# Performance work log

Measured on AMD Instinct MI355X. Metric: run time of the kernel, lower is better.

Reference implementation:

```python
import jax, jax.numpy as jnp
import numpy as np

N_NODES = 50000
N_EDGES = 1600000
HIDDEN = 64
HEADS = 8
EPS = 1e-16  # matches PyG segment-softmax denominator epsilon


def setup_inputs() -> dict:
    key = jax.random.key(0)
    ks = jax.random.split(key, 8)
    node_features = jax.random.normal(ks[0], (N_NODES,), dtype=jnp.float32)
    edge_index = jax.random.randint(ks[1], (2, N_EDGES), 0, N_NODES, dtype=jnp.int64)
    cycle_mask = jax.random.uniform(ks[2], (N_EDGES,), dtype=jnp.float32)
    # feature_proj: Linear(1, HIDDEN)
    W_proj = jax.random.normal(ks[3], (HIDDEN, 1), dtype=jnp.float32) * 0.5
    b_proj = jax.random.normal(ks[4], (HIDDEN,), dtype=jnp.float32) * 0.1
    # attention_net: Linear(2*HIDDEN+1, HEADS)
    fan_in = 2 * HIDDEN + 1
    W_att = jax.random.normal(ks[5], (HEADS, fan_in), dtype=jnp.float32) / np.sqrt(fan_in)
    b_att = jax.random.normal(ks[6], (HEADS,), dtype=jnp.float32) * 0.1
    cycle_penalty = jnp.full((HEADS,), -1.0, dtype=jnp.float32)
    min_sum_scaler = jnp.array([0.8], dtype=jnp.float32)
    return {
        "node_features": node_features,
        "cycle_mask": cycle_mask,
        "W_proj": W_proj,
        "b_proj": b_proj,
        "W_att": W_att,
        "b_att": b_att,
        "cycle_penalty": cycle_penalty,
        "min_sum_scaler": min_sum_scaler,
        "edge_index": edge_index,
    }


def reference(node_features, cycle_mask, W_proj, b_proj, W_att, b_att,
              cycle_penalty, min_sum_scaler, edge_index):
    src = edge_index[0]
    dst = edge_index[1]
    n = node_features.shape[0]
    w = W_proj[:, 0]  # [H]
    # per-edge projected features: [E, H]
    x_src = node_features[src][:, None] * w[None, :] + b_proj
    x_dst = node_features[dst][:, None] * w[None, :] + b_proj
    att_input = jnp.concatenate([x_src, x_dst, cycle_mask[:, None]], axis=-1)  # [E, 2H+1]
    raw = att_input @ W_att.T + b_att  # [E, heads]
    raw = jnp.where(raw >= 0, raw, 0.2 * raw)  # leaky_relu(0.2)
    raw = raw + cycle_mask[:, None] * cycle_penalty
    # segment softmax over edges grouped by dst
    seg_max = jax.ops.segment_max(raw, dst, num_segments=n)  # [N, heads]
    e = jnp.exp(raw - seg_max[dst])
    seg_sum = jax.ops.segment_sum(e, dst, num_segments=n)
    attn = e / (seg_sum[dst] + EPS)  # [E, heads]
    mean_attn = attn.mean(axis=-1)  # [E]
    messages = node_features[src] * mean_attn * min_sum_scaler[0]
    out = jax.ops.segment_sum(messages, dst, num_segments=n)
    return out
```

## Files before the change

### kernel.cpp

```cpp
#include <hip/hip_runtime.h>

#define N_NODES 50000
#define N_EDGES 1600000
#define HEADS 8
#define HIDDEN 64
#define FAN_IN (2*HIDDEN + 1)
#define EPSF 1e-16f

#define BBITS 8
#define BSIZE 256
#define BH 128
#define NB 196
#define NRB (NB * 2)
#define NSB 512
#define EPB 3125
#define NTS 256
#define NTR 512
#define CAPB 9216
#define CAP2 5120

#define CUR_OFF   0
#define PAY_OFF   4096
#define DL_OFF    (PAY_OFF + (size_t)NB * CAPB * 8)
#define WS_NEEDED (DL_OFF + (size_t)NB * CAPB)

__global__ __launch_bounds__(NTS) void k_scatter(const int* __restrict__ ei,
                                                 const float* __restrict__ cmask,
                                                 const float* __restrict__ nf,
                                                 int* __restrict__ cur,
                                                 float2* __restrict__ pay,
                                                 unsigned char* __restrict__ dl8) {
    __shared__ float          cmb[EPB];
    __shared__ int            pr[EPB];
    __shared__ unsigned short inv[EPB];
    __shared__ int            histL[NB];
    __shared__ int            emitoff[NB];
    __shared__ int            wsum[4];
    const int t = threadIdx.x, blk = blockIdx.x;
    const int e0 = blk * EPB;

    if (t < NB) histL[t] = 0;
    __syncthreads();

    for (int i = t; i < EPB; i += NTS) {
        const int dv = ei[N_EDGES + e0 + i];
        cmb[i] = cmask[e0 + i];
        const int bkt = ((unsigned)dv) >> BBITS;
        const int rank = atomicAdd(&histL[bkt], 1);
        pr[i] = (bkt << 20) | ((dv & (BSIZE - 1)) << 12) | rank;
    }
    __syncthreads();

    const int h = (t < NB) ? histL[t] : 0;
    int x = h;
    #pragma unroll
    for (int d = 1; d < 64; d <<= 1) {
        const int v = __shfl_up(x, d, 64);
        if ((t & 63) >= d) x += v;
    }
    if ((t & 63) == 63) wsum[t >> 6] = x;
    __syncthreads();
    int off = 0;
    #pragma unroll
    for (int w = 0; w < 4; ++w) if (w < (t >> 6)) off += wsum[w];
    const int lstart_t = off + x - h;

    int gb = 0;
    if (t < NB && h > 0) gb = atomicAdd(&cur[t], h);
    __syncthreads();
    if (t < NB) {
        emitoff[t] = t * CAPB + gb - lstart_t;
        histL[t]   = lstart_t;
    }
    __syncthreads();

    for (int i = t; i < EPB; i += NTS) {
        const int u = pr[i];
        inv[histL[u >> 20] + (u & 0xFFF)] = (unsigned short)i;
    }
    __syncthreads();

    for (int p = t; p < EPB; p += NTS) {
        const int i = inv[p];
        const int u = pr[i];
        const int bkt = u >> 20;
        const int g = emitoff[bkt] + p;
        if (g < (bkt + 1) * CAPB) {
            const int sv = ei[e0 + i];
            pay[g] = make_float2(nf[sv], cmb[i]);
            dl8[g] = (unsigned char)((u >> 12) & (BSIZE - 1));
        }
    }
}

__global__ __launch_bounds__(NTR) void k_reduce(const float* __restrict__ nf,
                                                const float* __restrict__ Wp,
                                                const float* __restrict__ bp,
                                                const float* __restrict__ Wa,
                                                const float* __restrict__ ba,
                                                const float* __restrict__ cp,
                                                const float* __restrict__ sc,
                                                const int* __restrict__ cur,
                                                const float2* __restrict__ pay,
                                                const unsigned char* __restrict__ dl8,
                                                float* __restrict__ out) {
    __shared__ float2        pbuf[CAP2];
    __shared__ unsigned char dl_l[CAPB];
    __shared__ int           histN[BH];
    __shared__ int           noff[BH + 1];
    __shared__ float         FD[BH];
    __shared__ float         cstl[40];
    const int t = threadIdx.x, b = blockIdx.x;
    const int bkt = b >> 1, half = b & 1;

    {
        const int k = t >> 6, j = t & 63;
        const float* row = Wa + k * FAN_IN;
        const float w = Wp[j], bb = bp[j];
        const float r1 = row[j], r2 = row[HIDDEN + j];
        float a1 = w * r1, a2 = w * r2, d = bb * (r1 + r2);
        #pragma unroll
        for (int s = 32; s > 0; s >>= 1) {
            a1 += __shfl_xor(a1, s);
            a2 += __shfl_xor(a2, s);
            d  += __shfl_xor(d, s);
        }
        if (j == 0) {
            cstl[k]      = a1;
            cstl[8 + k]  = a2;
            cstl[16 + k] = row[2 * HIDDEN];
            cstl[24 + k] = d + ba[k];
            cstl[32 + k] = cp[k];
        }
    }

    const int i0 = bkt * CAPB;
    const int len = min(cur[bkt], CAPB);

    if (t < BH) {
        histN[t] = 0;
        const int n = bkt * BSIZE + half * BH + t;
        FD[t] = (n < N_NODES) ? nf[n] : 0.f;
    }
    if (t == 0) noff[0] = 0;
    __syncthreads();

    for (int idx = t; idx < len; idx += NTR) {
        const int d8 = dl8[i0 + idx];
        dl_l[idx] = (unsigned char)d8;
        if ((d8 >> 7) == half) atomicAdd(&histN[d8 & (BH - 1)], 1);
    }
    __syncthreads();
    if (t < BH) noff[t + 1] = histN[t];
    __syncthreads();
    for (int d = 1; d < BH; d <<= 1) {
        int v = 0;
        if (t < BH && t >= d) v = noff[t + 1 - d];
        __syncthreads();
        if (t < BH && t >= d) noff[t + 1] += v;
        __syncthreads();
    }
    if (t < BH) histN[t] = noff[t];
    __syncthreads();

    for (int idx = t; idx < len; idx += NTR) {
        const int d8 = dl_l[idx];
        if ((d8 >> 7) == half) {
            const int p = atomicAdd(&histN[d8 & (BH - 1)], 1);
            if (p < CAP2) pbuf[p] = pay[i0 + idx];
        }
    }
    __syncthreads();

    float A1[8], A2[8], CC[8], DD[8], PP[8];
    #pragma unroll
    for (int k = 0; k < 8; ++k) {
        A1[k] = cstl[k];      A2[k] = cstl[8 + k];  CC[k] = cstl[16 + k];
        DD[k] = cstl[24 + k]; PP[k] = cstl[32 + k];
    }
    const int j = t >> 2, par = t & 3;
    const int n = bkt * BSIZE + half * BH + j;
    const int lo = min(noff[j], CAP2), hi = min(noff[j + 1], CAP2);
    const float fd = FD[j];
    float as[8], at[8];
    #pragma unroll
    for (int k = 0; k < 8; ++k) { as[k] = 0.f; at[k] = 0.f; }
    for (int i = lo + par; i < hi; i += 4) {
        const float2 p = pbuf[i];
        #pragma unroll
        for (int k = 0; k < 8; ++k) {
            float r = p.x * A1[k] + fd * A2[k] + p.y * CC[k] + DD[k];
            r = (r >= 0.f) ? r : 0.2f * r;
            r += p.y * PP[k];
            const float ev = __expf(r);
            as[k] += ev;
            at[k] += p.x * ev;
        }
    }
    #pragma unroll
    for (int k = 0; k < 8; ++k) {
        as[k] += __shfl_xor(as[k], 1);
        at[k] += __shfl_xor(at[k], 1);
        as[k] += __shfl_xor(as[k], 2);
        at[k] += __shfl_xor(at[k], 2);
    }
    if (par == 0 && n < N_NODES) {
        float acc = 0.f;
        #pragma unroll
        for (int k = 0; k < 8; ++k) acc += at[k] / (as[k] + EPSF);
        out[n] = acc * 0.125f * sc[0];
    }
}

__global__ __launch_bounds__(256) void cagat_edge_atomic(
    const float* __restrict__ nf, const float* __restrict__ cmask,
    const float* __restrict__ Wp, const float* __restrict__ bp,
    const float* __restrict__ Wa, const float* __restrict__ ba,
    const float* __restrict__ cp, const int* __restrict__ ei,
    float* __restrict__ S, float* __restrict__ T) {
    __shared__ float A1[HEADS], A2[HEADS], CC[HEADS], DD[HEADS], PP[HEADS];
    const int t = threadIdx.x;
    if (t < HEADS) {
        const float* row = Wa + t * FAN_IN;
        float a1 = 0.f, a2 = 0.f, d = 0.f;
        for (int h = 0; h < HIDDEN; ++h) {
            float w = Wp[h], b = bp[h];
            a1 += w * row[h]; a2 += w * row[HIDDEN + h];
            d += b * (row[h] + row[HIDDEN + h]);
        }
        A1[t] = a1; A2[t] = a2; CC[t] = row[2*HIDDEN]; DD[t] = d + ba[t]; PP[t] = cp[t];
    }
    __syncthreads();
    const int e = blockIdx.x * 256 + t;
    if (e >= N_EDGES) return;
    const int src = ei[e], dst = ei[N_EDGES + e];
    const float fs = nf[src], fd = nf[dst], c = cmask[e];
    #pragma unroll
    for (int k = 0; k < HEADS; ++k) {
        float r = fs * A1[k] + fd * A2[k] + c * CC[k] + DD[k];
        r = (r >= 0.f) ? r : 0.2f * r;
        r += c * PP[k];
        float ev = __expf(r);
        atomicAdd(S + dst * HEADS + k, ev);
        atomicAdd(T + dst * HEADS + k, fs * ev);
    }
}

__global__ __launch_bounds__(256) void cagat_node_atomic(
    const float* __restrict__ S, const float* __restrict__ T,
    const float* __restrict__ scaler, float* __restrict__ out) {
    const int n = blockIdx.x * 256 + threadIdx.x;
    if (n >= N_NODES) return;
    float acc = 0.f;
    #pragma unroll
    for (int k = 0; k < HEADS; ++k)
        acc += T[n * HEADS + k] / (S[n * HEADS + k] + EPSF);
    out[n] = acc * 0.125f * scaler[0];
}

extern "C" void kernel_launch(void* const* d_in, const int* in_sizes, int n_in,
                              void* d_out, int out_size, void* d_ws, size_t ws_size,
                              hipStream_t stream) {
    const float* nf    = (const float*)d_in[0];
    const float* cmask = (const float*)d_in[1];
    const float* Wp    = (const float*)d_in[2];
    const float* bp    = (const float*)d_in[3];
    const float* Wa    = (const float*)d_in[4];
    const float* ba    = (const float*)d_in[5];
    const float* cp    = (const float*)d_in[6];
    const float* sc    = (const float*)d_in[7];
    const int*   ei    = (const int*)d_in[8];

    char* ws = (char*)d_ws;

    if (ws_size >= WS_NEEDED) {
        int*           cur = (int*)(ws + CUR_OFF);
        float2*        pay = (float2*)(ws + PAY_OFF);
        unsigned char* dl  = (unsigned char*)(ws + DL_OFF);

        hipMemsetAsync(cur, 0, NB * sizeof(int), stream);
        k_scatter<<<NSB, NTS, 0, stream>>>(ei, cmask, nf, cur, pay, dl);
        k_reduce<<<NRB, NTR, 0, stream>>>(nf, Wp, bp, Wa, ba, cp, sc, cur,
                                          pay, dl, (float*)d_out);
    } else {
        float* S = (float*)d_ws;
        float* T = S + (size_t)N_NODES * HEADS;
        hipMemsetAsync(d_ws, 0, (size_t)N_NODES * HEADS * 2 * sizeof(float), stream);
        cagat_edge_atomic<<<(N_EDGES + 255) / 256, 256, 0, stream>>>(
            nf, cmask, Wp, bp, Wa, ba, cp, ei, S, T);
        cagat_node_atomic<<<(N_NODES + 255) / 256, 256, 0, stream>>>(
            S, T, sc, (float*)d_out);
    }
}
```

Measured before the change: 133.4 us.

## Pack edge payload to fp16 pairs and split reduce into quarter-buckets

The intermediate edge payload (source feature, cycle mask) is stored as two fp16 values packed into 32 bits instead of a float2, halving payload traffic between the scatter and reduce kernels. The scatter kernel uses twice as many blocks with fewer edges each, and the reduce kernel splits each 256-node bucket into four 64-node quarters, with 8 threads per node and a wave-shuffle prefix scan replacing the barrier-based scan. This raises parallelism but each reduce block rereads the full bucket's dl8 bytes four times, and fp16 rounding of node features and mask values adds precision error.

```diff
diff --git a/kernel.cpp b/kernel.cpp
--- a/kernel.cpp
+++ b/kernel.cpp
@@ -1,4 +1,5 @@
 #include <hip/hip_runtime.h>
+#include <hip/hip_fp16.h>
 
 #define N_NODES 50000
 #define N_EDGES 1600000
@@ -9,26 +10,32 @@
 
 #define BBITS 8
 #define BSIZE 256
-#define BH 128
 #define NB 196
-#define NRB (NB * 2)
-#define NSB 512
-#define EPB 3125
+#define NSB 1024
+#define EPB 1563
 #define NTS 256
-#define NTR 512
+#define QS 64
+#define NQB (NB * 4)
+#define NTQ 512
 #define CAPB 9216
-#define CAP2 5120
+#define CAPQ 2816
 
 #define CUR_OFF   0
 #define PAY_OFF   4096
-#define DL_OFF    (PAY_OFF + (size_t)NB * CAPB * 8)
+#define DL_OFF    (PAY_OFF + (size_t)NB * CAPB * 4)
 #define WS_NEEDED (DL_OFF + (size_t)NB * CAPB)
+
+__device__ __forceinline__ unsigned pack16(float fs, float cm) {
+    const unsigned short a = __half_as_ushort(__float2half_rn(fs));
+    const unsigned short b = __half_as_ushort(__float2half_rn(cm));
+    return (unsigned)a | ((unsigned)b << 16);
+}
 
 __global__ __launch_bounds__(NTS) void k_scatter(const int* __restrict__ ei,
                                                  const float* __restrict__ cmask,
                                                  const float* __restrict__ nf,
                                                  int* __restrict__ cur,
-                                                 float2* __restrict__ pay,
+                                                 unsigned* __restrict__ pay,
                                                  unsigned char* __restrict__ dl8) {
     __shared__ float          cmb[EPB];
     __shared__ int            pr[EPB];
@@ -38,11 +45,12 @@
     __shared__ int            wsum[4];
     const int t = threadIdx.x, blk = blockIdx.x;
     const int e0 = blk * EPB;
+    const int ecnt = min(EPB, N_EDGES - e0);
 
     if (t < NB) histL[t] = 0;
     __syncthreads();
 
-    for (int i = t; i < EPB; i += NTS) {
+    for (int i = t; i < ecnt; i += NTS) {
         const int dv = ei[N_EDGES + e0 + i];
         cmb[i] = cmask[e0 + i];
         const int bkt = ((unsigned)dv) >> BBITS;
@@ -74,26 +82,26 @@
     }
     __syncthreads();
 
-    for (int i = t; i < EPB; i += NTS) {
+    for (int i = t; i < ecnt; i += NTS) {
         const int u = pr[i];
         inv[histL[u >> 20] + (u & 0xFFF)] = (unsigned short)i;
     }
     __syncthreads();
 
-    for (int p = t; p < EPB; p += NTS) {
+    for (int p = t; p < ecnt; p += NTS) {
         const int i = inv[p];
         const int u = pr[i];
         const int bkt = u >> 20;
         const int g = emitoff[bkt] + p;
         if (g < (bkt + 1) * CAPB) {
             const int sv = ei[e0 + i];
-            pay[g] = make_float2(nf[sv], cmb[i]);
+            pay[g] = pack16(nf[sv], cmb[i]);
             dl8[g] = (unsigned char)((u >> 12) & (BSIZE - 1));
         }
     }
 }
 
-__global__ __launch_bounds__(NTR) void k_reduce(const float* __restrict__ nf,
+__global__ __launch_bounds__(NTQ) void k_reduce(const float* __restrict__ nf,
                                                 const float* __restrict__ Wp,
                                                 const float* __restrict__ bp,
                                                 const float* __restrict__ Wa,
@@ -101,17 +109,17 @@
                                                 const float* __restrict__ cp,
                                                 const float* __restrict__ sc,
                                                 const int* __restrict__ cur,
-                                                const float2* __restrict__ pay,
+                                                const unsigned* __restrict__ pay,
                                                 const unsigned char* __restrict__ dl8,
                                                 float* __restrict__ out) {
-    __shared__ float2        pbuf[CAP2];
+    __shared__ unsigned      pbuf[CAPQ];
     __shared__ unsigned char dl_l[CAPB];
-    __shared__ int           histN[BH];
-    __shared__ int           noff[BH + 1];
-    __shared__ float         FD[BH];
+    __shared__ int           histN[QS];
+    __shared__ int           noff[QS + 1];
+    __shared__ float         FD[QS];
     __shared__ float         cstl[40];
     const int t = threadIdx.x, b = blockIdx.x;
-    const int bkt = b >> 1, half = b & 1;
+    const int bkt = b >> 2, q = b & 3;
 
     {
         const int k = t >> 6, j = t & 63;
@@ -137,37 +145,39 @@
     const int i0 = bkt * CAPB;
     const int len = min(cur[bkt], CAPB);
 
-    if (t < BH) {
+    if (t < QS) {
         histN[t] = 0;
-        const int n = bkt * BSIZE + half * BH + t;
+        const int n = bkt * BSIZE + q * QS + t;
         FD[t] = (n < N_NODES) ? nf[n] : 0.f;
     }
-    if (t == 0) noff[0] = 0;
-    __syncthreads();
-
-    for (int idx = t; idx < len; idx += NTR) {
+    __syncthreads();
+
+    for (int idx = t; idx < len; idx += NTQ) {
         const int d8 = dl8[i0 + idx];
         dl_l[idx] = (unsigned char)d8;
-        if ((d8 >> 7) == half) atomicAdd(&histN[d8 & (BH - 1)], 1);
-    }
-    __syncthreads();
-    if (t < BH) noff[t + 1] = histN[t];
-    __syncthreads();
-    for (int d = 1; d < BH; d <<= 1) {
-        int v = 0;
-        if (t < BH && t >= d) v = noff[t + 1 - d];
-        __syncthreads();
-        if (t < BH && t >= d) noff[t + 1] += v;
-        __syncthreads();
-    }
-    if (t < BH) histN[t] = noff[t];
-    __syncthreads();
-
-    for (int idx = t; idx < len; idx += NTR) {
+        if ((d8 >> 6) == q) atomicAdd(&histN[d8 & (QS - 1)], 1);
+    }
+    __syncthreads();
+
+    if (t < QS) {
+        const int v = histN[t];
+        int inc = v;
+        #pragma unroll
+        for (int d = 1; d < 64; d <<= 1) {
+            const int u = __shfl_up(inc, d, 64);
+            if (t >= d) inc += u;
+        }
+        noff[t + 1] = inc;
+        if (t == 0) noff[0] = 0;
+        histN[t] = inc - v;
+    }
+    __syncthreads();
+
+    for (int idx = t; idx < len; idx += NTQ) {
         const int d8 = dl_l[idx];
-        if ((d8 >> 7) == half) {
-            const int p = atomicAdd(&histN[d8 & (BH - 1)], 1);
-            if (p < CAP2) pbuf[p] = pay[i0 + idx];
+        if ((d8 >> 6) == q) {
+            const int p = atomicAdd(&histN[d8 & (QS - 1)], 1);
+            if (p < CAPQ) pbuf[p] = pay[i0 + idx];
         }
     }
     __syncthreads();
@@ -178,23 +188,25 @@
         A1[k] = cstl[k];      A2[k] = cstl[8 + k];  CC[k] = cstl[16 + k];
         DD[k] = cstl[24 + k]; PP[k] = cstl[32 + k];
     }
-    const int j = t >> 2, par = t & 3;
-    const int n = bkt * BSIZE + half * BH + j;
-    const int lo = min(noff[j], CAP2), hi = min(noff[j + 1], CAP2);
+    const int j = t >> 3, par = t & 7;
+    const int n = bkt * BSIZE + q * QS + j;
+    const int lo = min(noff[j], CAPQ), hi = min(noff[j + 1], CAPQ);
     const float fd = FD[j];
     float as[8], at[8];
     #pragma unroll
     for (int k = 0; k < 8; ++k) { as[k] = 0.f; at[k] = 0.f; }
-    for (int i = lo + par; i < hi; i += 4) {
-        const float2 p = pbuf[i];
+    for (int i = lo + par; i < hi; i += 8) {
+        const unsigned u = pbuf[i];
+        const float fs = __half2float(__ushort_as_half((unsigned short)(u & 0xFFFF)));
+        const float c  = __half2float(__ushort_as_half((unsigned short)(u >> 16)));
         #pragma unroll
         for (int k = 0; k < 8; ++k) {
-            float r = p.x * A1[k] + fd * A2[k] + p.y * CC[k] + DD[k];
+            float r = fs * A1[k] + fd * A2[k] + c * CC[k] + DD[k];
             r = (r >= 0.f) ? r : 0.2f * r;
-            r += p.y * PP[k];
+            r += c * PP[k];
             const float ev = __expf(r);
             as[k] += ev;
-            at[k] += p.x * ev;
+            at[k] += fs * ev;
         }
     }
     #pragma unroll
@@ -203,6 +215,8 @@
         at[k] += __shfl_xor(at[k], 1);
         as[k] += __shfl_xor(as[k], 2);
         at[k] += __shfl_xor(at[k], 2);
+        as[k] += __shfl_xor(as[k], 4);
+        at[k] += __shfl_xor(at[k], 4);
     }
     if (par == 0 && n < N_NODES) {
         float acc = 0.f;
@@ -275,12 +289,12 @@
 
     if (ws_size >= WS_NEEDED) {
         int*           cur = (int*)(ws + CUR_OFF);
-        float2*        pay = (float2*)(ws + PAY_OFF);
+        unsigned*      pay = (unsigned*)(ws + PAY_OFF);
         unsigned char* dl  = (unsigned char*)(ws + DL_OFF);
 
         hipMemsetAsync(cur, 0, NB * sizeof(int), stream);
         k_scatter<<<NSB, NTS, 0, stream>>>(ei, cmask, nf, cur, pay, dl);
-        k_reduce<<<NRB, NTR, 0, stream>>>(nf, Wp, bp, Wa, ba, cp, sc, cur,
+        k_reduce<<<NQB, NTQ, 0, stream>>>(nf, Wp, bp, Wa, ba, cp, sc, cur,
                                           pay, dl, (float*)d_out);
     } else {
         float* S = (float*)d_ws;
```

Result: slower. 150.6 us (+12.9%).

## Pack edge payload as fp16 pairs and use wave-shuffle prefix scan

Applied to the files above, without the earlier changes.

The per-edge payload (source feature, cycle mask) is stored as two fp16 values packed in 32 bits instead of a float2. This halves payload traffic through the workspace and halves the shared-memory staging in the reduce kernel. The source gather is moved into the first pass of the scatter kernel, and the barrier-heavy shared-memory prefix scan in reduce is replaced by a wave shuffle scan. The cost is fp16 rounding of node features and mask values, which may raise error beyond tolerance. A leftover no-op histN assignment also remains.

```diff
diff --git a/kernel.cpp b/kernel.cpp
--- a/kernel.cpp
+++ b/kernel.cpp
@@ -1,4 +1,5 @@
 #include <hip/hip_runtime.h>
+#include <hip/hip_fp16.h>
 
 #define N_NODES 50000
 #define N_EDGES 1600000
@@ -21,16 +22,22 @@
 
 #define CUR_OFF   0
 #define PAY_OFF   4096
-#define DL_OFF    (PAY_OFF + (size_t)NB * CAPB * 8)
+#define DL_OFF    (PAY_OFF + (size_t)NB * CAPB * 4)
 #define WS_NEEDED (DL_OFF + (size_t)NB * CAPB)
+
+__device__ __forceinline__ unsigned pack16(float fs, float cm) {
+    const unsigned short a = __half_as_ushort(__float2half_rn(fs));
+    const unsigned short b = __half_as_ushort(__float2half_rn(cm));
+    return (unsigned)a | ((unsigned)b << 16);
+}
 
 __global__ __launch_bounds__(NTS) void k_scatter(const int* __restrict__ ei,
                                                  const float* __restrict__ cmask,
                                                  const float* __restrict__ nf,
                                                  int* __restrict__ cur,
-                                                 float2* __restrict__ pay,
+                                                 unsigned* __restrict__ pay,
                                                  unsigned char* __restrict__ dl8) {
-    __shared__ float          cmb[EPB];
+    __shared__ unsigned       pk[EPB];
     __shared__ int            pr[EPB];
     __shared__ unsigned short inv[EPB];
     __shared__ int            histL[NB];
@@ -43,8 +50,10 @@
     __syncthreads();
 
     for (int i = t; i < EPB; i += NTS) {
+        const int sv = ei[e0 + i];
         const int dv = ei[N_EDGES + e0 + i];
-        cmb[i] = cmask[e0 + i];
+        const float cv = cmask[e0 + i];
+        pk[i] = pack16(nf[sv], cv);
         const int bkt = ((unsigned)dv) >> BBITS;
         const int rank = atomicAdd(&histL[bkt], 1);
         pr[i] = (bkt << 20) | ((dv & (BSIZE - 1)) << 12) | rank;
@@ -86,8 +95,7 @@
         const int bkt = u >> 20;
         const int g = emitoff[bkt] + p;
         if (g < (bkt + 1) * CAPB) {
-            const int sv = ei[e0 + i];
-            pay[g] = make_float2(nf[sv], cmb[i]);
+            pay[g] = pk[i];
             dl8[g] = (unsigned char)((u >> 12) & (BSIZE - 1));
         }
     }
@@ -101,10 +109,10 @@
                                                 const float* __restrict__ cp,
                                                 const float* __restrict__ sc,
                                                 const int* __restrict__ cur,
-                                                const float2* __restrict__ pay,
+                                                const unsigned* __restrict__ pay,
                                                 const unsigned char* __restrict__ dl8,
                                                 float* __restrict__ out) {
-    __shared__ float2        pbuf[CAP2];
+    __shared__ unsigned      pbuf[CAP2];
     __shared__ unsigned char dl_l[CAPB];
     __shared__ int           histN[BH];
     __shared__ int           noff[BH + 1];
@@ -151,15 +159,25 @@
         if ((d8 >> 7) == half) atomicAdd(&histN[d8 & (BH - 1)], 1);
     }
     __syncthreads();
-    if (t < BH) noff[t + 1] = histN[t];
-    __syncthreads();
-    for (int d = 1; d < BH; d <<= 1) {
-        int v = 0;
-        if (t < BH && t >= d) v = noff[t + 1 - d];
-        __syncthreads();
-        if (t < BH && t >= d) noff[t + 1] += v;
-        __syncthreads();
-    }
+
+    if (t < BH) {
+        const int v = histN[t];
+        int inc = v;
+        #pragma unroll
+        for (int d = 1; d < 64; d <<= 1) {
+            const int u = __shfl_up(inc, d, 64);
+            if ((t & 63) >= d) inc += u;
+        }
+        noff[t + 1] = inc;
+    }
+    __syncthreads();
+    if (t < BH) {
+        int v = noff[t + 1];
+        if (t >= 64) v += noff[64];
+        noff[t + 1] = v;
+        histN[t] = v - ((t < BH) ? (noff[t + 1] - noff[t + 1]) : 0);
+    }
+    __syncthreads();
     if (t < BH) histN[t] = noff[t];
     __syncthreads();
 
@@ -186,15 +204,17 @@
     #pragma unroll
     for (int k = 0; k < 8; ++k) { as[k] = 0.f; at[k] = 0.f; }
     for (int i = lo + par; i < hi; i += 4) {
-        const float2 p = pbuf[i];
+        const unsigned u = pbuf[i];
+        const float fs = __half2float(__ushort_as_half((unsigned short)(u & 0xFFFF)));
+        const float c  = __half2float(__ushort_as_half((unsigned short)(u >> 16)));
         #pragma unroll
         for (int k = 0; k < 8; ++k) {
-            float r = p.x * A1[k] + fd * A2[k] + p.y * CC[k] + DD[k];
+            float r = fs * A1[k] + fd * A2[k] + c * CC[k] + DD[k];
             r = (r >= 0.f) ? r : 0.2f * r;
-            r += p.y * PP[k];
+            r += c * PP[k];
             const float ev = __expf(r);
             as[k] += ev;
-            at[k] += p.x * ev;
+            at[k] += fs * ev;
         }
     }
     #pragma unroll
@@ -275,7 +295,7 @@
 
     if (ws_size >= WS_NEEDED) {
         int*           cur = (int*)(ws + CUR_OFF);
-        float2*        pay = (float2*)(ws + PAY_OFF);
+        unsigned*      pay = (unsigned*)(ws + PAY_OFF);
         unsigned char* dl  = (unsigned char*)(ws + DL_OFF);
 
         hipMemsetAsync(cur, 0, NB * sizeof(int), stream);
```

After: 131.0 us. Within noise of the previous version (-1.8%).

## Pack dst-local index into fp16 cycle mask payload, drop local sort in scatter

Applied to the files above, without the earlier changes.

The cycle mask is stored as fp16 in the low half of the payload's second float, with the 8-bit destination-local index packed in the high half. This removes the separate dl8 byte array and its extra global reads and writes. The scatter kernel no longer sorts edges locally before emitting; each edge writes directly at its bucket offset plus its atomic rank, and it now runs with 512 threads. The reduce kernel's prefix scan becomes a wave shuffle, but it must read the 8-byte payload twice instead of one byte, and fp16 rounding of the cycle mask slightly changes numerics.

```diff
diff --git a/kernel.cpp b/kernel.cpp
--- a/kernel.cpp
+++ b/kernel.cpp
@@ -1,4 +1,5 @@
 #include <hip/hip_runtime.h>
+#include <hip/hip_fp16.h>
 
 #define N_NODES 50000
 #define N_EDGES 1600000
@@ -14,28 +15,29 @@
 #define NRB (NB * 2)
 #define NSB 512
 #define EPB 3125
-#define NTS 256
+#define NTS 512
 #define NTR 512
 #define CAPB 9216
 #define CAP2 5120
 
 #define CUR_OFF   0
 #define PAY_OFF   4096
-#define DL_OFF    (PAY_OFF + (size_t)NB * CAPB * 8)
-#define WS_NEEDED (DL_OFF + (size_t)NB * CAPB)
+#define WS_NEEDED (PAY_OFF + (size_t)NB * CAPB * 8)
+
+__device__ __forceinline__ float packY(float cm, int dl) {
+    const unsigned u = ((unsigned)dl << 16) |
+                       (unsigned)__half_as_ushort(__float2half_rn(cm));
+    return __uint_as_float(u);
+}
 
 __global__ __launch_bounds__(NTS) void k_scatter(const int* __restrict__ ei,
                                                  const float* __restrict__ cmask,
                                                  const float* __restrict__ nf,
                                                  int* __restrict__ cur,
-                                                 float2* __restrict__ pay,
-                                                 unsigned char* __restrict__ dl8) {
-    __shared__ float          cmb[EPB];
-    __shared__ int            pr[EPB];
-    __shared__ unsigned short inv[EPB];
-    __shared__ int            histL[NB];
-    __shared__ int            emitoff[NB];
-    __shared__ int            wsum[4];
+                                                 float2* __restrict__ pay) {
+    __shared__ int pr[EPB];
+    __shared__ int histL[NB];
+    __shared__ int emitoff[NB];
     const int t = threadIdx.x, blk = blockIdx.x;
     const int e0 = blk * EPB;
 
@@ -44,51 +46,28 @@
 
     for (int i = t; i < EPB; i += NTS) {
         const int dv = ei[N_EDGES + e0 + i];
-        cmb[i] = cmask[e0 + i];
         const int bkt = ((unsigned)dv) >> BBITS;
         const int rank = atomicAdd(&histL[bkt], 1);
         pr[i] = (bkt << 20) | ((dv & (BSIZE - 1)) << 12) | rank;
     }
     __syncthreads();
 
-    const int h = (t < NB) ? histL[t] : 0;
-    int x = h;
-    #pragma unroll
-    for (int d = 1; d < 64; d <<= 1) {
-        const int v = __shfl_up(x, d, 64);
-        if ((t & 63) >= d) x += v;
-    }
-    if ((t & 63) == 63) wsum[t >> 6] = x;
-    __syncthreads();
-    int off = 0;
-    #pragma unroll
-    for (int w = 0; w < 4; ++w) if (w < (t >> 6)) off += wsum[w];
-    const int lstart_t = off + x - h;
-
-    int gb = 0;
-    if (t < NB && h > 0) gb = atomicAdd(&cur[t], h);
-    __syncthreads();
     if (t < NB) {
-        emitoff[t] = t * CAPB + gb - lstart_t;
-        histL[t]   = lstart_t;
+        const int h = histL[t];
+        const int gb = (h > 0) ? atomicAdd(&cur[t], h) : 0;
+        emitoff[t] = t * CAPB + gb;
     }
     __syncthreads();
 
     for (int i = t; i < EPB; i += NTS) {
         const int u = pr[i];
-        inv[histL[u >> 20] + (u & 0xFFF)] = (unsigned short)i;
-    }
-    __syncthreads();
-
-    for (int p = t; p < EPB; p += NTS) {
-        const int i = inv[p];
-        const int u = pr[i];
         const int bkt = u >> 20;
-        const int g = emitoff[bkt] + p;
+        const int g = emitoff[bkt] + (u & 0xFFF);
         if (g < (bkt + 1) * CAPB) {
             const int sv = ei[e0 + i];
-            pay[g] = make_float2(nf[sv], cmb[i]);
-            dl8[g] = (unsigned char)((u >> 12) & (BSIZE - 1));
+            const float fs = nf[sv];
+            const float cm = cmask[e0 + i];
+            pay[g] = make_float2(fs, packY(cm, (u >> 12) & (BSIZE - 1)));
         }
     }
 }
@@ -102,14 +81,12 @@
                                                 const float* __restrict__ sc,
                                                 const int* __restrict__ cur,
                                                 const float2* __restrict__ pay,
-                                                const unsigned char* __restrict__ dl8,
                                                 float* __restrict__ out) {
-    __shared__ float2        pbuf[CAP2];
-    __shared__ unsigned char dl_l[CAPB];
-    __shared__ int           histN[BH];
-    __shared__ int           noff[BH + 1];
-    __shared__ float         FD[BH];
-    __shared__ float         cstl[40];
+    __shared__ float2 pbuf[CAP2];
+    __shared__ int    histN[BH];
+    __shared__ int    noff[BH + 1];
+    __shared__ float  FD[BH];
+    __shared__ float  cstl[40];
     const int t = threadIdx.x, b = blockIdx.x;
     const int bkt = b >> 1, half = b & 1;
 
@@ -146,28 +123,33 @@
     __syncthreads();
 
     for (int idx = t; idx < len; idx += NTR) {
-        const int d8 = dl8[i0 + idx];
-        dl_l[idx] = (unsigned char)d8;
-        if ((d8 >> 7) == half) atomicAdd(&histN[d8 & (BH - 1)], 1);
-    }
-    __syncthreads();
-    if (t < BH) noff[t + 1] = histN[t];
-    __syncthreads();
-    for (int d = 1; d < BH; d <<= 1) {
-        int v = 0;
-        if (t < BH && t >= d) v = noff[t + 1 - d];
-        __syncthreads();
-        if (t < BH && t >= d) noff[t + 1] += v;
-        __syncthreads();
-    }
+        const int dl = (int)(__float_as_uint(pay[i0 + idx].y) >> 16) & (BSIZE - 1);
+        if ((dl >> 7) == half) atomicAdd(&histN[dl & (BH - 1)], 1);
+    }
+    __syncthreads();
+
+    if (t < BH) {
+        const int v = histN[t];
+        int inc = v;
+        #pragma unroll
+        for (int d = 1; d < 64; d <<= 1) {
+            const int u = __shfl_up(inc, d, 64);
+            if ((t & 63) >= d) inc += u;
+        }
+        noff[t + 1] = inc;
+    }
+    __syncthreads();
+    if (t >= 64 && t < BH) noff[t + 1] += noff[64];
+    __syncthreads();
     if (t < BH) histN[t] = noff[t];
     __syncthreads();
 
     for (int idx = t; idx < len; idx += NTR) {
-        const int d8 = dl_l[idx];
-        if ((d8 >> 7) == half) {
-            const int p = atomicAdd(&histN[d8 & (BH - 1)], 1);
-            if (p < CAP2) pbuf[p] = pay[i0 + idx];
+        const float2 p = pay[i0 + idx];
+        const int dl = (int)(__float_as_uint(p.y) >> 16) & (BSIZE - 1);
+        if ((dl >> 7) == half) {
+            const int pos = atomicAdd(&histN[dl & (BH - 1)], 1);
+            if (pos < CAP2) pbuf[pos] = p;
         }
     }
     __syncthreads();
@@ -187,14 +169,17 @@
     for (int k = 0; k < 8; ++k) { as[k] = 0.f; at[k] = 0.f; }
     for (int i = lo + par; i < hi; i += 4) {
         const float2 p = pbuf[i];
+        const float fs = p.x;
+        const float c  = __half2float(
+            __ushort_as_half((unsigned short)(__float_as_uint(p.y) & 0xFFFF)));
         #pragma unroll
         for (int k = 0; k < 8; ++k) {
-            float r = p.x * A1[k] + fd * A2[k] + p.y * CC[k] + DD[k];
+            float r = fs * A1[k] + fd * A2[k] + c * CC[k] + DD[k];
             r = (r >= 0.f) ? r : 0.2f * r;
-            r += p.y * PP[k];
+            r += c * PP[k];
             const float ev = __expf(r);
             as[k] += ev;
-            at[k] += p.x * ev;
+            at[k] += fs * ev;
         }
     }
     #pragma unroll
@@ -274,14 +259,13 @@
     char* ws = (char*)d_ws;
 
     if (ws_size >= WS_NEEDED) {
-        int*           cur = (int*)(ws + CUR_OFF);
-        float2*        pay = (float2*)(ws + PAY_OFF);
-        unsigned char* dl  = (unsigned char*)(ws + DL_OFF);
+        int*    cur = (int*)(ws + CUR_OFF);
+        float2* pay = (float2*)(ws + PAY_OFF);
 
         hipMemsetAsync(cur, 0, NB * sizeof(int), stream);
-        k_scatter<<<NSB, NTS, 0, stream>>>(ei, cmask, nf, cur, pay, dl);
+        k_scatter<<<NSB, NTS, 0, stream>>>(ei, cmask, nf, cur, pay);
         k_reduce<<<NRB, NTR, 0, stream>>>(nf, Wp, bp, Wa, ba, cp, sc, cur,
-                                          pay, dl, (float*)d_out);
+                                          pay, (float*)d_out);
     } else {
         float* S = (float*)d_ws;
         float* T = S + (size_t)N_NODES * HEADS;
```

Result: no change. 131.0 us (-1.8%).
